# Kernel optimization log

Hardware: AMD Instinct MI355X
Metric: run time of the kernel (lower is better)

The kernel has to match this reference:

```python
import jax, jax.numpy as jnp
from jax import lax
import numpy as np


def tridiagonal_solve(K, f):
    """Batched Thomas-algorithm solve of A(K) u = f.

    K: [..., m] diffusion coefficient at m grid points.
    f: broadcastable to [..., m-1] right-hand side.
    Returns u: [..., m-1].
    """
    n = K.shape[-1] - 1  # number of unknowns
    h2 = 1.0 / (n * n)
    f = jnp.broadcast_to(f, (*K.shape[:-1], n))

    denom0 = 2.0 * K[..., 0] + K[..., 1]
    c0 = -K[..., 1] / denom0  # [...]
    u0 = f[..., 0] / denom0

    # Forward elimination sweep, j = 1 .. n-2, as a scan over the grid axis.
    Kj = jnp.moveaxis(K[..., 1:n - 1], -1, 0)   # [n-2, ...] = K[..., j]
    Kj1 = jnp.moveaxis(K[..., 2:n], -1, 0)      # [n-2, ...] = K[..., j+1]
    fj = jnp.moveaxis(f[..., 1:n - 1], -1, 0)   # [n-2, ...]

    def fwd_step(carry, x):
        c_prev, u_prev = carry
        kj, kj1, fv = x
        denom = kj + kj1 + kj * c_prev
        c = -kj1 / denom
        u = (fv + kj * u_prev) / denom
        return (c, u), (c, u)

    _, (cs, us) = lax.scan(fwd_step, (c0, u0), (Kj, Kj1, fj))
    c_all = jnp.concatenate([c0[None], cs], axis=0)  # [n-1, ...] indices 0..n-2
    u_all = jnp.concatenate([u0[None], us], axis=0)  # [n-1, ...]

    Kn1 = K[..., n - 1]
    u_last = (f[..., n - 1] + Kn1 * u_all[-1]) / (Kn1 + Kn1 * c_all[-1])  # u[n-1]

    # Back substitution: u[j] -= c[j] * u[j+1], j = n-2 .. 0 (reverse scan).
    def bwd_step(u_next, x):
        cj, uj = x
        u_new = uj - cj * u_next
        return u_new, u_new

    _, u_head = lax.scan(bwd_step, u_last, (c_all, u_all), reverse=True)  # [n-1, ...]
    u_full = jnp.concatenate([u_head, u_last[None]], axis=0)  # [n, ...]
    return h2 * jnp.moveaxis(u_full, 0, -1)


def setup_inputs() -> dict:
    key = jax.random.key(0)
    k1, k2 = jax.random.split(key)
    B, M = 16384, 1024  # batch, grid points (n = M - 1 unknowns)
    alpha = jax.random.normal(k1, (B, M), dtype=jnp.float32)
    f_rhs = jax.random.normal(k2, (M - 1,), dtype=jnp.float32)
    return {"alpha": alpha, "f_rhs": f_rhs}


def reference(alpha, f_rhs):
    # DiffusionModel1d.forward: u = A(exp(alpha))^{-1} f_rhs
    return tridiagonal_solve(jnp.exp(alpha), f_rhs)
```

## Files before the change

### kernel.cpp

```cpp
#include <hip/hip_runtime.h>
#include <math.h>


constexpr int BT   = 16384;
constexpr int MPTS = 1024;
constexpr int NU   = 1023;
constexpr int CS   = 16;
constexpr int WPB  = 4;

__device__ __forceinline__ float frcp(float x) {
    float r = __builtin_amdgcn_rcpf(x);
    r = fmaf(r, fmaf(-x, r, 1.0f), r);
    return r;
}
__device__ __forceinline__ double drcp(double x) {
    double r = __builtin_amdgcn_rcp(x);
    r = fma(r, fma(-x, r, 1.0), r);
    return r;
}
__device__ __forceinline__ int sw(int j) { return j + (j >> 5); }

__global__ __launch_bounds__(WPB * 64, 4)
void pt_kernel(const float* __restrict__ alpha,
               const float* __restrict__ f_rhs,
               float* __restrict__ out) {
    const int t    = threadIdx.x;
    const int lane = t & 63;
    const int w    = t >> 6;
    const int row  = blockIdx.x * WPB + w;
    const int s    = lane * CS;

    __shared__ float f_lds[1056];
    __shared__ float ostage[WPB][1056];

    const float h2 = (float)(1.0 / (1023.0 * 1023.0));
    for (int i = t; i < NU; i += WPB * 64) f_lds[sw(i)] = h2 * f_rhs[i];
    if (t == 0) f_lds[sw(1023)] = 0.0f;

    const float* arow = alpha + (size_t)row * MPTS;
    float kf[CS + 1];
    #pragma unroll
    for (int q = 0; q < 4; ++q) {
        const float4 v = *reinterpret_cast<const float4*>(arow + s + 4 * q);
        kf[4 * q + 0] = expf(v.x);
        kf[4 * q + 1] = expf(v.y);
        kf[4 * q + 2] = expf(v.z);
        kf[4 * q + 3] = expf(v.w);
    }
    {
        float kx = (lane < 63) ? arow[s + CS] : 0.0f;
        kf[CS] = expf(kx);
    }
    if (lane == 63) kf[15] = 0.0f;

    __syncthreads();

    float cF = (lane == 0) ? 1.0f : 0.0f, uF = 0.0f, vF = 1.0f;
    float uRv = 0.0f, vRv = 1.0f, wRv = 0.0f;
    #pragma unroll
    for (int i = 0; i < CS; ++i) {
        {
            const float kc = kf[i], kn = kf[i + 1];
            const float b  = kc + kn;
            const float f  = f_lds[sw(s + i)];
            const float den = fmaf(kc, cF, b);
            const float r   = frcp(den);
            float ci = -kn * r;
            const float ui = fmaf(kc, uF, f) * r;
            const float vi = (kc * vF) * r;
            if (i == CS - 1) ci = (lane == 63) ? 0.0f : ci;
            cF = ci; uF = ui; vF = vi;
        }
        {
            const int ir = CS - 1 - i;
            float kc = kf[ir];
            const float kn = kf[ir + 1];
            float b = kc + kn;
            if (ir == 0) {
                b  = (lane == 0) ? (b + kc) : b;
                kc = (lane == 0) ? 0.0f : kc;
            }
            const float f  = f_lds[sw(s + ir)];
            const float den = fmaf(-kn, wRv, b);
            const float r   = frcp(den);
            const float ui = fmaf(kn, uRv, f) * r;
            const float vi = (kn * vRv) * r;
            const float wi = kc * r;
            uRv = ui; vRv = vi; wRv = wi;
        }
    }
    const float De_f = uF,  Ae_f = vF,  Be_f = -cF;
    const float Ds_f = uRv, Bs_f = vRv, As_f = wRv;

    const double Ds = (double)Ds_f, As = (double)As_f, Bs = (double)Bs_f;
    const double De = (double)De_f, Ae = (double)Ae_f, Be = (double)Be_f;
    double m00 = Bs;
    double m01 = fma(Bs, De, -(Ds * Be));
    double m02 = Ds;
    double m11 = fma(Bs, Ae, -(As * Be));
    double m12 = As;
    double m21 = -Be;

    #pragma unroll
    for (int dlt = 1; dlt < 64; dlt <<= 1) {
        const bool val = (lane + dlt) < 64;
        double b00 = __shfl_down(m00, dlt); b00 = val ? b00 : 1.0;
        double b01 = __shfl_down(m01, dlt); b01 = val ? b01 : 0.0;
        double b02 = __shfl_down(m02, dlt); b02 = val ? b02 : 0.0;
        double b11 = __shfl_down(m11, dlt); b11 = val ? b11 : 1.0;
        double b12 = __shfl_down(m12, dlt); b12 = val ? b12 : 0.0;
        double b21 = __shfl_down(m21, dlt); b21 = val ? b21 : 0.0;
        const double n00 = m00 * b00;
        const double n01 = fma(m00, b01, fma(m01, b11, m02 * b21));
        const double n02 = fma(m00, b02, fma(m01, b12, m02));
        const double n11 = fma(m11, b11, m12 * b21);
        const double n12 = fma(m11, b12, m12);
        const double n21 = fma(m21, b11, b21);
        const double n22 = fma(m21, b12, 1.0);
        const double rn = drcp(n22);
        m00 = n00 * rn; m01 = n01 * rn; m02 = n02 * rn;
        m11 = n11 * rn; m12 = n12 * rn; m21 = n21 * rn;
    }
    const double alf = m02;
    const double bet = m12;
    double alfn = __shfl_down(alf, 1); alfn = (lane == 63) ? 0.0 : alfn;
    double betn = __shfl_down(bet, 1); betn = (lane == 63) ? 0.0 : betn;

    const double tt = drcp(fma(-Be, betn, 1.0));
    const double dl = fma(Be, alfn, De) * tt;
    const double gm = Ae * tt;

    double X = dl, G = gm;
    #pragma unroll
    for (int dlt = 1; dlt < 64; dlt <<= 1) {
        double bx = __shfl_up(X, dlt);
        double bg = __shfl_up(G, dlt);
        const bool val = lane >= dlt;
        bx = val ? bx : 0.0;
        bg = val ? bg : 1.0;
        X = fma(G, bx, X);
        G = G * bg;
    }
    double xp = __shfl_up(X, 1);
    const double uLd = (lane == 0) ? 0.0 : xp;
    const double Y   = fma(bet, uLd, alf);
    double yn = __shfl_down(Y, 1);
    const double uRd = (lane == 63) ? 0.0 : yn;

    const float uL = (float)uLd;
    const float uR = (float)uRd;
    float c3[CS], u3[CS];
    {
        float cp = (lane == 0) ? 1.0f : 0.0f, up = 0.0f;
        #pragma unroll
        for (int i = 0; i < CS; ++i) {
            const float kc = kf[i], kn = kf[i + 1];
            const float b  = kc + kn;
            float f = f_lds[sw(s + i)];
            if (i == 0)      f = fmaf(kf[0],  uL, f);
            if (i == CS - 1) f = fmaf(kf[CS], uR, f);
            const float den = fmaf(kc, cp, b);
            const float r   = frcp(den);
            const float ci = -kn * r;
            const float ui = fmaf(kc, up, f) * r;
            c3[i] = ci; u3[i] = ui;
            cp = ci; up = ui;
        }
    }
    float* ost = ostage[w];
    {
        float un = u3[CS - 1];
        ost[sw(s + CS - 1)] = un;
        #pragma unroll
        for (int i = CS - 2; i >= 0; --i) {
            un = fmaf(-c3[i], un, u3[i]);
            ost[sw(s + i)] = un;
        }
    }
    __syncthreads();

    float* orow = out + (size_t)row * NU;
    #pragma unroll
    for (int it = 0; it < 16; ++it) {
        const int c = it * 64 + lane;
        if (c < NU) orow[c] = ost[sw(c)];
    }
}

extern "C" void kernel_launch(void* const* d_in, const int* in_sizes, int n_in,
                              void* d_out, int out_size, void* d_ws, size_t ws_size,
                              hipStream_t stream) {
    const float* alpha = (const float*)d_in[0];
    const float* f_rhs = (const float*)d_in[1];
    float* out = (float*)d_out;

    dim3 grid(BT / WPB), block(WPB * 64);
    pt_kernel<<<grid, block, 0, stream>>>(alpha, f_rhs, out);
}
```

Before: 39.73 us.

## Process two rows per wavefront with 32-element chunks split into two sub-chains

Each wavefront now solves two rows, one per half-wave, and each lane owns 32 grid points instead of 16. Each lane's chunk is handled as two interleaved 16-point sub-chains, which are merged algebraically before a shorter 5-step double-precision shuffle scan. The final sweep reuses the reciprocals from the first pass instead of recomputing them. This cuts the per-row cost of the serial log-depth shuffle scans and the redundant third elimination pass. In exchange it raises register pressure (occupancy hint lowered from 4 to 3) and serialises the output staging through LDS across the two rows.

```diff
diff --git a/kernel.cpp b/kernel.cpp
--- a/kernel.cpp
+++ b/kernel.cpp
@@ -5,8 +5,11 @@
 constexpr int BT   = 16384;
 constexpr int MPTS = 1024;
 constexpr int NU   = 1023;
-constexpr int CS   = 16;
+constexpr int CS   = 32;
+constexpr int HS   = 16;
+constexpr int NG   = 32;
 constexpr int WPB  = 4;
+constexpr int RPB  = WPB*2;
 
 __device__ __forceinline__ float frcp(float x) {
     float r = __builtin_amdgcn_rcpf(x);
@@ -20,15 +23,18 @@
 }
 __device__ __forceinline__ int sw(int j) { return j + (j >> 5); }
 
-__global__ __launch_bounds__(WPB * 64, 4)
+__global__ __launch_bounds__(WPB * 64, 3)
 void pt_kernel(const float* __restrict__ alpha,
                const float* __restrict__ f_rhs,
                float* __restrict__ out) {
     const int t    = threadIdx.x;
     const int lane = t & 63;
     const int w    = t >> 6;
-    const int row  = blockIdx.x * WPB + w;
-    const int s    = lane * CS;
+    const int g    = lane & 31;
+    const int h    = lane >> 5;
+    const int rowbase = blockIdx.x * RPB + w * 2;
+    const int row  = rowbase + h;
+    const int s    = g * CS;
 
     __shared__ float f_lds[1056];
     __shared__ float ostage[WPB][1056];
@@ -40,7 +46,7 @@
     const float* arow = alpha + (size_t)row * MPTS;
     float kf[CS + 1];
     #pragma unroll
-    for (int q = 0; q < 4; ++q) {
+    for (int q = 0; q < 8; ++q) {
         const float4 v = *reinterpret_cast<const float4*>(arow + s + 4 * q);
         kf[4 * q + 0] = expf(v.x);
         kf[4 * q + 1] = expf(v.y);
@@ -48,52 +54,94 @@
         kf[4 * q + 3] = expf(v.w);
     }
     {
-        float kx = (lane < 63) ? arow[s + CS] : 0.0f;
+        float kx = (g < NG - 1) ? arow[s + CS] : 0.0f;
         kf[CS] = expf(kx);
     }
-    if (lane == 63) kf[15] = 0.0f;
-
-    __syncthreads();
-
-    float cF = (lane == 0) ? 1.0f : 0.0f, uF = 0.0f, vF = 1.0f;
-    float uRv = 0.0f, vRv = 1.0f, wRv = 0.0f;
-    #pragma unroll
-    for (int i = 0; i < CS; ++i) {
+    if (g == NG - 1) kf[CS - 1] = 0.0f;
+
+    __syncthreads();
+
+    float rA[CS];
+    float cF1 = (g == 0) ? 1.0f : 0.0f, uF1 = 0.0f, vF1 = 1.0f;
+    float cF2 = 0.0f,                   uF2 = 0.0f, vF2 = 1.0f;
+    float u1r = 0.0f, v1r = 1.0f, w1r = 0.0f;
+    float u2r = 0.0f, v2r = 1.0f, w2r = 0.0f;
+    #pragma unroll
+    for (int i = 0; i < HS; ++i) {
         {
             const float kc = kf[i], kn = kf[i + 1];
             const float b  = kc + kn;
             const float f  = f_lds[sw(s + i)];
-            const float den = fmaf(kc, cF, b);
-            const float r   = frcp(den);
+            const float den = fmaf(kc, cF1, b);
+            const float r   = frcp(den);
+            rA[i] = r;
+            cF1 = -kn * r;
+            uF1 = fmaf(kc, uF1, f) * r;
+            vF1 = (kc * vF1) * r;
+        }
+        {
+            const int i2 = HS + i;
+            const float kc = kf[i2], kn = kf[i2 + 1];
+            const float b  = kc + kn;
+            const float f  = f_lds[sw(s + i2)];
+            const float den = fmaf(kc, cF2, b);
+            const float r   = frcp(den);
+            rA[i2] = r;
             float ci = -kn * r;
-            const float ui = fmaf(kc, uF, f) * r;
-            const float vi = (kc * vF) * r;
-            if (i == CS - 1) ci = (lane == 63) ? 0.0f : ci;
-            cF = ci; uF = ui; vF = vi;
-        }
-        {
-            const int ir = CS - 1 - i;
+            if (i2 == CS - 1) ci = (g == NG - 1) ? 0.0f : ci;
+            uF2 = fmaf(kc, uF2, f) * r;
+            vF2 = (kc * vF2) * r;
+            cF2 = ci;
+        }
+        {
+            const int ir = HS - 1 - i;
             float kc = kf[ir];
             const float kn = kf[ir + 1];
             float b = kc + kn;
             if (ir == 0) {
-                b  = (lane == 0) ? (b + kc) : b;
-                kc = (lane == 0) ? 0.0f : kc;
+                b  = (g == 0) ? (b + kc) : b;
+                kc = (g == 0) ? 0.0f : kc;
             }
             const float f  = f_lds[sw(s + ir)];
-            const float den = fmaf(-kn, wRv, b);
-            const float r   = frcp(den);
-            const float ui = fmaf(kn, uRv, f) * r;
-            const float vi = (kn * vRv) * r;
-            const float wi = kc * r;
-            uRv = ui; vRv = vi; wRv = wi;
-        }
-    }
-    const float De_f = uF,  Ae_f = vF,  Be_f = -cF;
-    const float Ds_f = uRv, Bs_f = vRv, As_f = wRv;
-
-    const double Ds = (double)Ds_f, As = (double)As_f, Bs = (double)Bs_f;
-    const double De = (double)De_f, Ae = (double)Ae_f, Be = (double)Be_f;
+            const float den = fmaf(-kn, w1r, b);
+            const float r   = frcp(den);
+            u1r = fmaf(kn, u1r, f) * r;
+            v1r = (kn * v1r) * r;
+            w1r = kc * r;
+        }
+        {
+            const int ir = CS - 1 - i;
+            const float kc = kf[ir];
+            const float kn = kf[ir + 1];
+            const float b  = kc + kn;
+            const float f  = f_lds[sw(s + ir)];
+            const float den = fmaf(-kn, w2r, b);
+            const float r   = frcp(den);
+            u2r = fmaf(kn, u2r, f) * r;
+            v2r = (kn * v2r) * r;
+            w2r = kc * r;
+        }
+    }
+
+    const double De1 = (double)uF1, Ae1 = (double)vF1, Be1 = -(double)cF1;
+    const double De2 = (double)uF2, Ae2 = (double)vF2, Be2 = -(double)cF2;
+    const double Ds1 = (double)u1r, Bs1 = (double)v1r, As1 = (double)w1r;
+    const double Ds2 = (double)u2r, Bs2 = (double)v2r, As2 = (double)w2r;
+
+    const double q  = drcp(fma(-As2, Be1, 1.0));
+    const double P0 = q * fma(As2, De1, Ds2);
+    const double PL = q * (As2 * Ae1);
+    const double PR = q * Bs2;
+    const double L0 = fma(Be1, P0, De1);
+    const double LL = fma(Be1, PL, Ae1);
+    const double LR = Be1 * PR;
+    const double Ds = fma(Bs1, P0, Ds1);
+    const double As = fma(Bs1, PL, As1);
+    const double Bs = Bs1 * PR;
+    const double De = fma(Ae2, L0, De2);
+    const double Ae = Ae2 * LL;
+    const double Be = fma(Ae2, LR, Be2);
+
     double m00 = Bs;
     double m01 = fma(Bs, De, -(Ds * Be));
     double m02 = Ds;
@@ -102,8 +150,8 @@
     double m21 = -Be;
 
     #pragma unroll
-    for (int dlt = 1; dlt < 64; dlt <<= 1) {
-        const bool val = (lane + dlt) < 64;
+    for (int dlt = 1; dlt < NG; dlt <<= 1) {
+        const bool val = (g + dlt) < NG;
         double b00 = __shfl_down(m00, dlt); b00 = val ? b00 : 1.0;
         double b01 = __shfl_down(m01, dlt); b01 = val ? b01 : 0.0;
         double b02 = __shfl_down(m02, dlt); b02 = val ? b02 : 0.0;
@@ -123,8 +171,8 @@
     }
     const double alf = m02;
     const double bet = m12;
-    double alfn = __shfl_down(alf, 1); alfn = (lane == 63) ? 0.0 : alfn;
-    double betn = __shfl_down(bet, 1); betn = (lane == 63) ? 0.0 : betn;
+    double alfn = __shfl_down(alf, 1); alfn = (g == NG - 1) ? 0.0 : alfn;
+    double betn = __shfl_down(bet, 1); betn = (g == NG - 1) ? 0.0 : betn;
 
     const double tt = drcp(fma(-Be, betn, 1.0));
     const double dl = fma(Be, alfn, De) * tt;
@@ -132,58 +180,96 @@
 
     double X = dl, G = gm;
     #pragma unroll
-    for (int dlt = 1; dlt < 64; dlt <<= 1) {
+    for (int dlt = 1; dlt < NG; dlt <<= 1) {
         double bx = __shfl_up(X, dlt);
         double bg = __shfl_up(G, dlt);
-        const bool val = lane >= dlt;
+        const bool val = g >= dlt;
         bx = val ? bx : 0.0;
         bg = val ? bg : 1.0;
         X = fma(G, bx, X);
         G = G * bg;
     }
     double xp = __shfl_up(X, 1);
-    const double uLd = (lane == 0) ? 0.0 : xp;
+    const double uLd = (g == 0) ? 0.0 : xp;
     const double Y   = fma(bet, uLd, alf);
     double yn = __shfl_down(Y, 1);
-    const double uRd = (lane == 63) ? 0.0 : yn;
-
-    const float uL = (float)uLd;
-    const float uR = (float)uRd;
-    float c3[CS], u3[CS];
-    {
-        float cp = (lane == 0) ? 1.0f : 0.0f, up = 0.0f;
-        #pragma unroll
-        for (int i = 0; i < CS; ++i) {
-            const float kc = kf[i], kn = kf[i + 1];
-            const float b  = kc + kn;
-            float f = f_lds[sw(s + i)];
-            if (i == 0)      f = fmaf(kf[0],  uL, f);
-            if (i == CS - 1) f = fmaf(kf[CS], uR, f);
-            const float den = fmaf(kc, cp, b);
-            const float r   = frcp(den);
-            const float ci = -kn * r;
-            const float ui = fmaf(kc, up, f) * r;
-            c3[i] = ci; u3[i] = ui;
-            cp = ci; up = ui;
-        }
-    }
+    const double uRd = (g == NG - 1) ? 0.0 : yn;
+
+    const double uMd  = fma(PL, uLd, fma(PR, uRd, P0));
+    const double uL1d = fma(LL, uLd, fma(LR, uRd, L0));
+    const float uL  = (float)uLd;
+    const float uM  = (float)uMd;
+    const float uL1 = (float)uL1d;
+    const float uR  = (float)uRd;
+
+    float u3[CS];
+    {
+        float up1 = 0.0f, up2 = 0.0f;
+        #pragma unroll
+        for (int i = 0; i < HS; ++i) {
+            {
+                float f = f_lds[sw(s + i)];
+                if (i == 0)      f = fmaf(kf[0],  uL, f);
+                if (i == HS - 1) f = fmaf(kf[HS], uM, f);
+                up1 = fmaf(kf[i], up1, f) * rA[i];
+                u3[i] = up1;
+                rA[i] = kf[i + 1] * rA[i];
+            }
+            {
+                const int i2 = HS + i;
+                float f = f_lds[sw(s + i2)];
+                if (i == 0)      f = fmaf(kf[HS], uL1, f);
+                if (i == HS - 1) f = fmaf(kf[CS], uR, f);
+                up2 = fmaf(kf[i2], up2, f) * rA[i2];
+                u3[i2] = up2;
+                rA[i2] = kf[i2 + 1] * rA[i2];
+            }
+        }
+    }
+    {
+        float un = u3[HS - 1];
+        #pragma unroll
+        for (int i = HS - 2; i >= 0; --i) {
+            un = fmaf(rA[i], un, u3[i]);
+            u3[i] = un;
+        }
+    }
+    {
+        float un = u3[CS - 1];
+        #pragma unroll
+        for (int i = CS - 2; i >= HS; --i) {
+            un = fmaf(rA[i], un, u3[i]);
+            u3[i] = un;
+        }
+    }
+
     float* ost = ostage[w];
-    {
-        float un = u3[CS - 1];
-        ost[sw(s + CS - 1)] = un;
-        #pragma unroll
-        for (int i = CS - 2; i >= 0; --i) {
-            un = fmaf(-c3[i], un, u3[i]);
-            ost[sw(s + i)] = un;
-        }
-    }
-    __syncthreads();
-
-    float* orow = out + (size_t)row * NU;
-    #pragma unroll
-    for (int it = 0; it < 16; ++it) {
-        const int c = it * 64 + lane;
-        if (c < NU) orow[c] = ost[sw(c)];
+    if (h == 0) {
+        #pragma unroll
+        for (int i = 0; i < CS; ++i) ost[sw(s + i)] = u3[i];
+    }
+    __syncthreads();
+    {
+        float* orow = out + (size_t)rowbase * NU;
+        #pragma unroll
+        for (int it = 0; it < 16; ++it) {
+            const int c = it * 64 + lane;
+            if (c < NU) orow[c] = ost[sw(c)];
+        }
+    }
+    __syncthreads();
+    if (h == 1) {
+        #pragma unroll
+        for (int i = 0; i < CS; ++i) ost[sw(s + i)] = u3[i];
+    }
+    __syncthreads();
+    {
+        float* orow = out + (size_t)(rowbase + 1) * NU;
+        #pragma unroll
+        for (int it = 0; it < 16; ++it) {
+            const int c = it * 64 + lane;
+            if (c < NU) orow[c] = ost[sw(c)];
+        }
     }
 }
 
@@ -194,6 +280,6 @@
     const float* f_rhs = (const float*)d_in[1];
     float* out = (float*)d_out;
 
-    dim3 grid(BT / WPB), block(WPB * 64);
+    dim3 grid(BT / RPB), block(WPB * 64);
     pt_kernel<<<grid, block, 0, stream>>>(alpha, f_rhs, out);
 }
```

New measurement: 38.77 us. 2.4% less time.

## Process two rows per wavefront with interleaved recurrences and LDS-staged coefficients

Applied to the files above, without the earlier changes.

Each wavefront now solves two batch rows and interleaves their forward/backward chunk recurrences and shuffle scans, so independent dependency chains can hide latency from rcp and cross-lane shuffles. The exp(alpha) coefficients are staged in LDS instead of registers, and that same buffer is reused for the output staging, which drops the block-wide barrier before the store. This costs more LDS traffic and register pressure from the doubled state, and halves the grid size, which may reduce occupancy or load balance.

```diff
diff --git a/kernel.cpp b/kernel.cpp
--- a/kernel.cpp
+++ b/kernel.cpp
@@ -7,6 +7,7 @@
 constexpr int NU   = 1023;
 constexpr int CS   = 16;
 constexpr int WPB  = 4;
+constexpr int RPB  = 8;
 
 __device__ __forceinline__ float frcp(float x) {
     float r = __builtin_amdgcn_rcpf(x);
@@ -20,170 +21,267 @@
 }
 __device__ __forceinline__ int sw(int j) { return j + (j >> 5); }
 
-__global__ __launch_bounds__(WPB * 64, 4)
+__global__ __launch_bounds__(256, 4)
 void pt_kernel(const float* __restrict__ alpha,
                const float* __restrict__ f_rhs,
                float* __restrict__ out) {
     const int t    = threadIdx.x;
     const int lane = t & 63;
     const int w    = t >> 6;
-    const int row  = blockIdx.x * WPB + w;
+    const int rowA = blockIdx.x * RPB + 2 * w;
+    const int rowB = rowA + 1;
     const int s    = lane * CS;
 
     __shared__ float f_lds[1056];
-    __shared__ float ostage[WPB][1056];
+    __shared__ float klds[RPB][1058];
 
     const float h2 = (float)(1.0 / (1023.0 * 1023.0));
-    for (int i = t; i < NU; i += WPB * 64) f_lds[sw(i)] = h2 * f_rhs[i];
+    for (int i = t; i < NU; i += 256) f_lds[sw(i)] = h2 * f_rhs[i];
     if (t == 0) f_lds[sw(1023)] = 0.0f;
 
-    const float* arow = alpha + (size_t)row * MPTS;
-    float kf[CS + 1];
-    #pragma unroll
-    for (int q = 0; q < 4; ++q) {
-        const float4 v = *reinterpret_cast<const float4*>(arow + s + 4 * q);
-        kf[4 * q + 0] = expf(v.x);
-        kf[4 * q + 1] = expf(v.y);
-        kf[4 * q + 2] = expf(v.z);
-        kf[4 * q + 3] = expf(v.w);
-    }
-    {
-        float kx = (lane < 63) ? arow[s + CS] : 0.0f;
-        kf[CS] = expf(kx);
-    }
-    if (lane == 63) kf[15] = 0.0f;
-
+    float* klA = klds[2 * w];
+    float* klB = klds[2 * w + 1];
+    {
+        const float* ar = alpha + (size_t)rowA * MPTS;
+        const float* br = alpha + (size_t)rowB * MPTS;
+        #pragma unroll
+        for (int q = 0; q < 4; ++q) {
+            const int j0 = s + 4 * q;
+            const float4 va = *reinterpret_cast<const float4*>(ar + j0);
+            const float4 vb = *reinterpret_cast<const float4*>(br + j0);
+            klA[sw(j0 + 0)] = expf(va.x); klA[sw(j0 + 1)] = expf(va.y);
+            klA[sw(j0 + 2)] = expf(va.z); klA[sw(j0 + 3)] = expf(va.w);
+            klB[sw(j0 + 0)] = expf(vb.x); klB[sw(j0 + 1)] = expf(vb.y);
+            klB[sw(j0 + 2)] = expf(vb.z); klB[sw(j0 + 3)] = expf(vb.w);
+        }
+        if (lane == 63) {
+            klA[sw(1023)] = 0.0f; klA[sw(1024)] = 1.0f;
+            klB[sw(1023)] = 0.0f; klB[sw(1024)] = 1.0f;
+        }
+    }
     __syncthreads();
 
-    float cF = (lane == 0) ? 1.0f : 0.0f, uF = 0.0f, vF = 1.0f;
-    float uRv = 0.0f, vRv = 1.0f, wRv = 0.0f;
+    const float k0A = klA[sw(s)], k16A = klA[sw(s + 16)];
+    const float k0B = klB[sw(s)], k16B = klB[sw(s + 16)];
+
+    float cFA = (lane == 0) ? 1.0f : 0.0f, uFA = 0.0f, vFA = 1.0f, kcFA = k0A;
+    float cFB = (lane == 0) ? 1.0f : 0.0f, uFB = 0.0f, vFB = 1.0f, kcFB = k0B;
+    float uRvA = 0.0f, vRvA = 1.0f, wRvA = 0.0f, knRA = k16A;
+    float uRvB = 0.0f, vRvB = 1.0f, wRvB = 0.0f, knRB = k16B;
     #pragma unroll
     for (int i = 0; i < CS; ++i) {
-        {
-            const float kc = kf[i], kn = kf[i + 1];
-            const float b  = kc + kn;
-            const float f  = f_lds[sw(s + i)];
-            const float den = fmaf(kc, cF, b);
+        const int j  = s + i;
+        const int jr = s + (CS - 1 - i);
+        const float fj = f_lds[sw(j)];
+        const float fr = f_lds[sw(jr)];
+        {
+            const float kn = klA[sw(j + 1)];
+            const float b  = kcFA + kn;
+            const float den = fmaf(kcFA, cFA, b);
             const float r   = frcp(den);
             float ci = -kn * r;
-            const float ui = fmaf(kc, uF, f) * r;
-            const float vi = (kc * vF) * r;
             if (i == CS - 1) ci = (lane == 63) ? 0.0f : ci;
-            cF = ci; uF = ui; vF = vi;
-        }
-        {
-            const int ir = CS - 1 - i;
-            float kc = kf[ir];
-            const float kn = kf[ir + 1];
-            float b = kc + kn;
-            if (ir == 0) {
-                b  = (lane == 0) ? (b + kc) : b;
-                kc = (lane == 0) ? 0.0f : kc;
+            uFA = fmaf(kcFA, uFA, fj) * r;
+            vFA = (kcFA * vFA) * r;
+            cFA = ci; kcFA = kn;
+        }
+        {
+            const float kn = klB[sw(j + 1)];
+            const float b  = kcFB + kn;
+            const float den = fmaf(kcFB, cFB, b);
+            const float r   = frcp(den);
+            float ci = -kn * r;
+            if (i == CS - 1) ci = (lane == 63) ? 0.0f : ci;
+            uFB = fmaf(kcFB, uFB, fj) * r;
+            vFB = (kcFB * vFB) * r;
+            cFB = ci; kcFB = kn;
+        }
+        {
+            const float kcr = klA[sw(jr)];
+            float b   = kcr + knRA;
+            float kcm = kcr;
+            if (i == CS - 1) {
+                b   = (lane == 0) ? (b + kcr) : b;
+                kcm = (lane == 0) ? 0.0f : kcr;
             }
-            const float f  = f_lds[sw(s + ir)];
-            const float den = fmaf(-kn, wRv, b);
-            const float r   = frcp(den);
-            const float ui = fmaf(kn, uRv, f) * r;
-            const float vi = (kn * vRv) * r;
-            const float wi = kc * r;
-            uRv = ui; vRv = vi; wRv = wi;
-        }
-    }
-    const float De_f = uF,  Ae_f = vF,  Be_f = -cF;
-    const float Ds_f = uRv, Bs_f = vRv, As_f = wRv;
-
-    const double Ds = (double)Ds_f, As = (double)As_f, Bs = (double)Bs_f;
-    const double De = (double)De_f, Ae = (double)Ae_f, Be = (double)Be_f;
-    double m00 = Bs;
-    double m01 = fma(Bs, De, -(Ds * Be));
-    double m02 = Ds;
-    double m11 = fma(Bs, Ae, -(As * Be));
-    double m12 = As;
-    double m21 = -Be;
+            const float den = fmaf(-knRA, wRvA, b);
+            const float r   = frcp(den);
+            uRvA = fmaf(knRA, uRvA, fr) * r;
+            vRvA = (knRA * vRvA) * r;
+            wRvA = kcm * r;
+            knRA = kcr;
+        }
+        {
+            const float kcr = klB[sw(jr)];
+            float b   = kcr + knRB;
+            float kcm = kcr;
+            if (i == CS - 1) {
+                b   = (lane == 0) ? (b + kcr) : b;
+                kcm = (lane == 0) ? 0.0f : kcr;
+            }
+            const float den = fmaf(-knRB, wRvB, b);
+            const float r   = frcp(den);
+            uRvB = fmaf(knRB, uRvB, fr) * r;
+            vRvB = (knRB * vRvB) * r;
+            wRvB = kcm * r;
+            knRB = kcr;
+        }
+    }
+
+    const double DsA = (double)uRvA, AsA = (double)wRvA, BsA = (double)vRvA;
+    const double DeA = (double)uFA,  AeA = (double)vFA,  BeA = -(double)cFA;
+    const double DsB = (double)uRvB, AsB = (double)wRvB, BsB = (double)vRvB;
+    const double DeB = (double)uFB,  AeB = (double)vFB,  BeB = -(double)cFB;
+
+    double mA00 = BsA, mA01 = fma(BsA, DeA, -(DsA * BeA)), mA02 = DsA;
+    double mA11 = fma(BsA, AeA, -(AsA * BeA)), mA12 = AsA, mA21 = -BeA;
+    double mB00 = BsB, mB01 = fma(BsB, DeB, -(DsB * BeB)), mB02 = DsB;
+    double mB11 = fma(BsB, AeB, -(AsB * BeB)), mB12 = AsB, mB21 = -BeB;
 
     #pragma unroll
     for (int dlt = 1; dlt < 64; dlt <<= 1) {
         const bool val = (lane + dlt) < 64;
-        double b00 = __shfl_down(m00, dlt); b00 = val ? b00 : 1.0;
-        double b01 = __shfl_down(m01, dlt); b01 = val ? b01 : 0.0;
-        double b02 = __shfl_down(m02, dlt); b02 = val ? b02 : 0.0;
-        double b11 = __shfl_down(m11, dlt); b11 = val ? b11 : 1.0;
-        double b12 = __shfl_down(m12, dlt); b12 = val ? b12 : 0.0;
-        double b21 = __shfl_down(m21, dlt); b21 = val ? b21 : 0.0;
-        const double n00 = m00 * b00;
-        const double n01 = fma(m00, b01, fma(m01, b11, m02 * b21));
-        const double n02 = fma(m00, b02, fma(m01, b12, m02));
-        const double n11 = fma(m11, b11, m12 * b21);
-        const double n12 = fma(m11, b12, m12);
-        const double n21 = fma(m21, b11, b21);
-        const double n22 = fma(m21, b12, 1.0);
-        const double rn = drcp(n22);
-        m00 = n00 * rn; m01 = n01 * rn; m02 = n02 * rn;
-        m11 = n11 * rn; m12 = n12 * rn; m21 = n21 * rn;
-    }
-    const double alf = m02;
-    const double bet = m12;
-    double alfn = __shfl_down(alf, 1); alfn = (lane == 63) ? 0.0 : alfn;
-    double betn = __shfl_down(bet, 1); betn = (lane == 63) ? 0.0 : betn;
-
-    const double tt = drcp(fma(-Be, betn, 1.0));
-    const double dl = fma(Be, alfn, De) * tt;
-    const double gm = Ae * tt;
-
-    double X = dl, G = gm;
+        double a00 = __shfl_down(mA00, dlt); a00 = val ? a00 : 1.0;
+        double b00 = __shfl_down(mB00, dlt); b00 = val ? b00 : 1.0;
+        double a01 = __shfl_down(mA01, dlt); a01 = val ? a01 : 0.0;
+        double b01 = __shfl_down(mB01, dlt); b01 = val ? b01 : 0.0;
+        double a02 = __shfl_down(mA02, dlt); a02 = val ? a02 : 0.0;
+        double b02 = __shfl_down(mB02, dlt); b02 = val ? b02 : 0.0;
+        double a11 = __shfl_down(mA11, dlt); a11 = val ? a11 : 1.0;
+        double b11 = __shfl_down(mB11, dlt); b11 = val ? b11 : 1.0;
+        double a12 = __shfl_down(mA12, dlt); a12 = val ? a12 : 0.0;
+        double b12 = __shfl_down(mB12, dlt); b12 = val ? b12 : 0.0;
+        double a21 = __shfl_down(mA21, dlt); a21 = val ? a21 : 0.0;
+        double b21 = __shfl_down(mB21, dlt); b21 = val ? b21 : 0.0;
+
+        const double nA00 = mA00 * a00;
+        const double nB00 = mB00 * b00;
+        const double nA01 = fma(mA00, a01, fma(mA01, a11, mA02 * a21));
+        const double nB01 = fma(mB00, b01, fma(mB01, b11, mB02 * b21));
+        const double nA02 = fma(mA00, a02, fma(mA01, a12, mA02));
+        const double nB02 = fma(mB00, b02, fma(mB01, b12, mB02));
+        const double nA11 = fma(mA11, a11, mA12 * a21);
+        const double nB11 = fma(mB11, b11, mB12 * b21);
+        const double nA12 = fma(mA11, a12, mA12);
+        const double nB12 = fma(mB11, b12, mB12);
+        const double nA21 = fma(mA21, a11, a21);
+        const double nB21 = fma(mB21, b11, b21);
+        const double nA22 = fma(mA21, a12, 1.0);
+        const double nB22 = fma(mB21, b12, 1.0);
+        const double rnA = drcp(nA22);
+        const double rnB = drcp(nB22);
+        mA00 = nA00 * rnA; mA01 = nA01 * rnA; mA02 = nA02 * rnA;
+        mA11 = nA11 * rnA; mA12 = nA12 * rnA; mA21 = nA21 * rnA;
+        mB00 = nB00 * rnB; mB01 = nB01 * rnB; mB02 = nB02 * rnB;
+        mB11 = nB11 * rnB; mB12 = nB12 * rnB; mB21 = nB21 * rnB;
+    }
+    const double alfA = mA02, betA = mA12;
+    const double alfB = mB02, betB = mB12;
+    double alfnA = __shfl_down(alfA, 1); alfnA = (lane == 63) ? 0.0 : alfnA;
+    double betnA = __shfl_down(betA, 1); betnA = (lane == 63) ? 0.0 : betnA;
+    double alfnB = __shfl_down(alfB, 1); alfnB = (lane == 63) ? 0.0 : alfnB;
+    double betnB = __shfl_down(betB, 1); betnB = (lane == 63) ? 0.0 : betnB;
+
+    const double ttA = drcp(fma(-BeA, betnA, 1.0));
+    const double ttB = drcp(fma(-BeB, betnB, 1.0));
+    const double dlA = fma(BeA, alfnA, DeA) * ttA;
+    const double dlB = fma(BeB, alfnB, DeB) * ttB;
+    const double gmA = AeA * ttA;
+    const double gmB = AeB * ttB;
+
+    double XA = dlA, GA = gmA, XB = dlB, GB = gmB;
     #pragma unroll
     for (int dlt = 1; dlt < 64; dlt <<= 1) {
-        double bx = __shfl_up(X, dlt);
-        double bg = __shfl_up(G, dlt);
+        double bxA = __shfl_up(XA, dlt);
+        double bxB = __shfl_up(XB, dlt);
+        double bgA = __shfl_up(GA, dlt);
+        double bgB = __shfl_up(GB, dlt);
         const bool val = lane >= dlt;
-        bx = val ? bx : 0.0;
-        bg = val ? bg : 1.0;
-        X = fma(G, bx, X);
-        G = G * bg;
-    }
-    double xp = __shfl_up(X, 1);
-    const double uLd = (lane == 0) ? 0.0 : xp;
-    const double Y   = fma(bet, uLd, alf);
-    double yn = __shfl_down(Y, 1);
-    const double uRd = (lane == 63) ? 0.0 : yn;
-
-    const float uL = (float)uLd;
-    const float uR = (float)uRd;
-    float c3[CS], u3[CS];
-    {
-        float cp = (lane == 0) ? 1.0f : 0.0f, up = 0.0f;
+        bxA = val ? bxA : 0.0;  bgA = val ? bgA : 1.0;
+        bxB = val ? bxB : 0.0;  bgB = val ? bgB : 1.0;
+        XA = fma(GA, bxA, XA);  GA = GA * bgA;
+        XB = fma(GB, bxB, XB);  GB = GB * bgB;
+    }
+    double xpA = __shfl_up(XA, 1);
+    double xpB = __shfl_up(XB, 1);
+    const double uLdA = (lane == 0) ? 0.0 : xpA;
+    const double uLdB = (lane == 0) ? 0.0 : xpB;
+    const double YA = fma(betA, uLdA, alfA);
+    const double YB = fma(betB, uLdB, alfB);
+    double ynA = __shfl_down(YA, 1);
+    double ynB = __shfl_down(YB, 1);
+    const double uRdA = (lane == 63) ? 0.0 : ynA;
+    const double uRdB = (lane == 63) ? 0.0 : ynB;
+
+    {
+        const float uL = (float)uLdA, uR = (float)uRdA;
+        float c3[CS], u3[CS];
+        float cp = (lane == 0) ? 1.0f : 0.0f, up = 0.0f, kc = k0A;
         #pragma unroll
         for (int i = 0; i < CS; ++i) {
-            const float kc = kf[i], kn = kf[i + 1];
+            const float kn = klA[sw(s + i + 1)];
             const float b  = kc + kn;
             float f = f_lds[sw(s + i)];
-            if (i == 0)      f = fmaf(kf[0],  uL, f);
-            if (i == CS - 1) f = fmaf(kf[CS], uR, f);
+            if (i == 0)      f = fmaf(k0A,  uL, f);
+            if (i == CS - 1) f = fmaf(k16A, uR, f);
             const float den = fmaf(kc, cp, b);
             const float r   = frcp(den);
             const float ci = -kn * r;
             const float ui = fmaf(kc, up, f) * r;
             c3[i] = ci; u3[i] = ui;
-            cp = ci; up = ui;
-        }
-    }
-    float* ost = ostage[w];
-    {
+            cp = ci; up = ui; kc = kn;
+        }
         float un = u3[CS - 1];
-        ost[sw(s + CS - 1)] = un;
+        klA[sw(s + CS - 1)] = un;
         #pragma unroll
         for (int i = CS - 2; i >= 0; --i) {
             un = fmaf(-c3[i], un, u3[i]);
-            ost[sw(s + i)] = un;
-        }
-    }
-    __syncthreads();
-
-    float* orow = out + (size_t)row * NU;
-    #pragma unroll
-    for (int it = 0; it < 16; ++it) {
-        const int c = it * 64 + lane;
-        if (c < NU) orow[c] = ost[sw(c)];
+            klA[sw(s + i)] = un;
+        }
+    }
+    asm volatile("s_waitcnt lgkmcnt(0)" ::: "memory");
+    {
+        float* orow = out + (size_t)rowA * NU;
+        #pragma unroll
+        for (int it = 0; it < 16; ++it) {
+            const int c = it * 64 + lane;
+            if (c < NU) orow[c] = klA[sw(c)];
+        }
+    }
+    {
+        const float uL = (float)uLdB, uR = (float)uRdB;
+        float c3[CS], u3[CS];
+        float cp = (lane == 0) ? 1.0f : 0.0f, up = 0.0f, kc = k0B;
+        #pragma unroll
+        for (int i = 0; i < CS; ++i) {
+            const float kn = klB[sw(s + i + 1)];
+            const float b  = kc + kn;
+            float f = f_lds[sw(s + i)];
+            if (i == 0)      f = fmaf(k0B,  uL, f);
+            if (i == CS - 1) f = fmaf(k16B, uR, f);
+            const float den = fmaf(kc, cp, b);
+            const float r   = frcp(den);
+            const float ci = -kn * r;
+            const float ui = fmaf(kc, up, f) * r;
+            c3[i] = ci; u3[i] = ui;
+            cp = ci; up = ui; kc = kn;
+        }
+        float un = u3[CS - 1];
+        klB[sw(s + CS - 1)] = un;
+        #pragma unroll
+        for (int i = CS - 2; i >= 0; --i) {
+            un = fmaf(-c3[i], un, u3[i]);
+            klB[sw(s + i)] = un;
+        }
+    }
+    asm volatile("s_waitcnt lgkmcnt(0)" ::: "memory");
+    {
+        float* orow = out + (size_t)rowB * NU;
+        #pragma unroll
+        for (int it = 0; it < 16; ++it) {
+            const int c = it * 64 + lane;
+            if (c < NU) orow[c] = klB[sw(c)];
+        }
     }
 }
 
@@ -194,6 +292,6 @@
     const float* f_rhs = (const float*)d_in[1];
     float* out = (float*)d_out;
 
-    dim3 grid(BT / WPB), block(WPB * 64);
+    dim3 grid(BT / RPB), block(WPB * 64);
     pt_kernel<<<grid, block, 0, stream>>>(alpha, f_rhs, out);
 }
```

New measurement: 42.29 us. 1.06x slower.
